# Kernel optimization log

Measured on AMD Instinct MI355X. Metric: run time of the kernel, lower is better.

The kernel has to match this reference:

```python
import jax, jax.numpy as jnp
import numpy as np

B, S, SE, D, H = 4, 1024, 256, 1536, 24
HD = D // H
EPS = 1e-5
STYLE_IDX = np.array([0, 0, 2, 2])  # expand_first: style stats of sample 0 -> {0,1}, sample 2 -> {2,3}


def adain(feat):
    # feat: [B,H,S,hd]; stats over seq dim (-2), unbiased var like torch
    m = feat.mean(axis=-2, keepdims=True)
    s = jnp.sqrt(feat.var(axis=-2, keepdims=True, ddof=1) + EPS)
    sm, ss = m[STYLE_IDX], s[STYLE_IDX]
    styled = (feat - m) / s * ss + sm
    # only batch indices 1 and 3 are restyled
    mask = jnp.array([0.0, 1.0, 0.0, 1.0], dtype=feat.dtype).reshape(B, 1, 1, 1)
    return feat * (1.0 - mask) + styled * mask


def heads(x):
    b, s, _ = x.shape
    return x.reshape(b, s, H, HD).transpose(0, 2, 1, 3)


def setup_inputs() -> dict:
    key = jax.random.key(0)
    ks = jax.random.split(key, 12)
    w = lambda k: jax.random.normal(k, (D, D), dtype=jnp.float32) * 0.02
    z = jnp.zeros((D,), dtype=jnp.float32)
    return {
        'hidden_states': jax.random.normal(ks[0], (B, S, D), dtype=jnp.float32),
        'encoder_hidden_states': jax.random.normal(ks[1], (B, SE, D), dtype=jnp.float32),
        'wq': w(ks[2]), 'bq': z, 'wk': w(ks[3]), 'bk': z, 'wv': w(ks[4]), 'bv': z,
        'awq': w(ks[5]), 'abq': z, 'awk': w(ks[6]), 'abk': z, 'awv': w(ks[7]), 'abv': z,
        'wo': w(ks[8]), 'bo': z, 'wao': w(ks[9]), 'bao': z,
    }


def reference(hidden_states, encoder_hidden_states, wq, bq, wk, bk, wv, bv,
              awq, abq, awk, abk, awv, abv, wo, bo, wao, bao):
    q = heads(hidden_states @ wq + bq)   # [B,H,S,hd]
    k = heads(hidden_states @ wk + bk)
    v = heads(hidden_states @ wv + bv)
    # adain_queries / adain_keys (adain_values=False)
    q = adain(q)
    k = adain(k)
    # share_attention: concat style K/V (scale=1.0 -> plain expand) along seq
    k = jnp.concatenate([k, k[STYLE_IDX]], axis=2)  # [B,H,2S,hd]
    v = jnp.concatenate([v, v[STYLE_IDX]], axis=2)
    # joint (text) streams
    eq = heads(encoder_hidden_states @ awq + abq)
    ek = heads(encoder_hidden_states @ awk + abk)
    ev = heads(encoder_hidden_states @ awv + abv)
    q = jnp.concatenate([q, eq], axis=2)   # [B,H,S+SE,hd]
    k = jnp.concatenate([k, ek], axis=2)   # [B,H,2S+SE,hd]
    v = jnp.concatenate([v, ev], axis=2)
    scale = 1.0 / np.sqrt(HD)
    logits = jnp.einsum('bhqd,bhkd->bhqk', q, k) * scale
    probs = jax.nn.softmax(logits, axis=-1)
    out = jnp.einsum('bhqk,bhkd->bhqd', probs, v)
    out = out.transpose(0, 2, 1, 3).reshape(B, -1, D)
    hid, enc = out[:, :S], out[:, S:]
    hid = hid @ wo + bo            # to_out[0] (to_out[1] is dropout/identity)
    enc = enc @ wao + bao          # to_add_out (context_pre_only=False)
    return hid, enc
```

## Files before the change

kernel.cpp:

```cpp
#include <hip/hip_runtime.h>
#include <hip/hip_bf16.h>


#define NB 4
#define NS 1024
#define NSE 256
#define ND 1536
#define NH 24
#define LK2 1280
#define SMAX 20.0f
#define LOG2E 1.44269504f

typedef short bf16x8 __attribute__((ext_vector_type(8)));
typedef float f32x4 __attribute__((ext_vector_type(4)));

struct WPtrs { const float* w[8]; };
struct B6    { const float* p[6]; };

__device__ __forceinline__ unsigned short f2bf(float x) {
  union { float f; unsigned u; } a; a.f = x;
  unsigned r = a.u + 0x7fffu + ((a.u >> 16) & 1u);
  return (unsigned short)(r >> 16);
}
__device__ __forceinline__ void split2(float x, unsigned short& h, unsigned short& l) {
  union { float f; unsigned u; } a; a.f = x;
  h = (unsigned short)(a.u >> 16);
  union { float f; unsigned u; } b; b.u = a.u & 0xffff0000u;
  union { float f; unsigned u; } c; c.f = x - b.f;
  l = (unsigned short)(c.u >> 16);
}

__device__ __forceinline__ void gload_lds16(const unsigned short* g, unsigned short* l) {
  __builtin_amdgcn_global_load_lds(
      (const __attribute__((address_space(1))) void*)g,
      (__attribute__((address_space(3))) void*)l, 16, 0, 0);
}

__global__ __launch_bounds__(256) void conv_split_all(
    const float* __restrict__ hs, const float* __restrict__ ehs,
    unsigned short* __restrict__ HSh, unsigned short* __restrict__ HSl,
    unsigned short* __restrict__ EHh, unsigned short* __restrict__ EHl)
{
  int i = blockIdx.x * 256 + threadIdx.x;
  const float4* src; ushort4 *dh, *dl; int j;
  if (i < 1572864) { src = (const float4*)hs; j = i; dh = (ushort4*)HSh; dl = (ushort4*)HSl; }
  else { j = i - 1572864; src = (const float4*)ehs; dh = (ushort4*)EHh; dl = (ushort4*)EHl; }
  float4 v = src[j];
  ushort4 h, lo;
  split2(v.x, h.x, lo.x); split2(v.y, h.y, lo.y);
  split2(v.z, h.z, lo.z); split2(v.w, h.w, lo.w);
  dh[j] = h; dl[j] = lo;
}

__global__ __launch_bounds__(256) void conv_wt_all(WPtrs wp,
                                                   unsigned short* __restrict__ Wsp)
{
  __shared__ float tile[32][33];
  const int z = blockIdx.z;
  const float* W = wp.w[z];
  unsigned short* Th = Wsp + (long)(2 * z) * 2359296;
  unsigned short* Tl = Th + 2359296;
  const int k0 = blockIdx.x * 32, n0 = blockIdx.y * 32;
  const int r = threadIdx.x >> 5, c = threadIdx.x & 31;
#pragma unroll
  for (int i = 0; i < 4; ++i)
    tile[r + 8 * i][c] = W[(long)(k0 + r + 8 * i) * ND + n0 + c];
  __syncthreads();
#pragma unroll
  for (int i = 0; i < 4; ++i) {
    float v = tile[c][r + 8 * i];
    long o = (long)(n0 + r + 8 * i) * ND + k0 + c;
    unsigned short h, l;
    split2(v, h, l);
    Th[o] = h; Tl[o] = l;
  }
}

__global__ __launch_bounds__(512, 2) void gemm_qk8(
    const unsigned short* __restrict__ HSh, const unsigned short* __restrict__ EHh,
    const unsigned short* __restrict__ Wsp, B6 biases,
    float* __restrict__ Qb, float* __restrict__ Kb,
    float* __restrict__ EQb, float* __restrict__ EKb)
{
  __shared__ unsigned short sA[2][256 * 32];
  __shared__ unsigned short sBh[2][256 * 32];
  __shared__ unsigned short sBl[2][256 * 32];

  const int lin = blockIdx.x;
  const int idx = (lin & 7) * 30 + (lin >> 3);
  const int z   = idx / 120;
  const int rem = idx % 120;
  const int xn  = rem / 20;
  const int ym  = rem % 20;
  const bool enc = ym >= 16;
  const int m0 = (enc ? (ym - 16) : ym) * 256;
  const int n0 = xn * 256;
  const int widx = z + (enc ? 3 : 0);
  const unsigned short* A  = enc ? EHh : HSh;
  const unsigned short* Bh = Wsp + (long)(2 * widx) * 2359296;
  const unsigned short* Bl = Bh + 2359296;
  float* C = z ? (enc ? EKb : Kb) : (enc ? EQb : Qb);
  const float* bias = biases.p[widx];

  const int t = threadIdx.x, w = t >> 6, l = t & 63;
  const int wm = w >> 2, wn = w & 3;

  const int lrow = l >> 2;
  const int swz  = (l & 3) ^ (lrow & 3);
  const unsigned short* gA0  = A  + (long)(m0 +       w * 16 + lrow) * ND + swz * 8;
  const unsigned short* gA1  = A  + (long)(m0 + 128 + w * 16 + lrow) * ND + swz * 8;
  const unsigned short* gBh0 = Bh + (long)(n0 +       w * 16 + lrow) * ND + swz * 8;
  const unsigned short* gBh1 = Bh + (long)(n0 + 128 + w * 16 + lrow) * ND + swz * 8;
  const unsigned short* gBl0 = Bl + (long)(n0 +       w * 16 + lrow) * ND + swz * 8;
  const unsigned short* gBl1 = Bl + (long)(n0 + 128 + w * 16 + lrow) * ND + swz * 8;

  const int fr = l & 15;
  const int ks = l >> 4;
  const int kx = ((ks ^ (fr & 3)) * 8);

  auto stage = [&](int kt, int bi) {
    const int k0 = kt * 32;
    gload_lds16(gA0  + k0, &sA [bi][(w * 16) * 32]);
    gload_lds16(gA1  + k0, &sA [bi][(128 + w * 16) * 32]);
    gload_lds16(gBh0 + k0, &sBh[bi][(w * 16) * 32]);
    gload_lds16(gBh1 + k0, &sBh[bi][(128 + w * 16) * 32]);
    gload_lds16(gBl0 + k0, &sBl[bi][(w * 16) * 32]);
    gload_lds16(gBl1 + k0, &sBl[bi][(128 + w * 16) * 32]);
  };

  f32x4 acc[8][4] = {};

  stage(0, 0);
  const int NT = ND / 32;
  for (int kt = 0; kt < NT; ++kt) {
    const int cur = kt & 1;
    stage((kt + 1) % NT, cur ^ 1);
    asm volatile("s_waitcnt vmcnt(6)" ::: "memory");
    __builtin_amdgcn_s_barrier();
    __builtin_amdgcn_sched_barrier(0);

    const unsigned short* pA  = &sA[cur][0];
    const unsigned short* pBhc = &sBh[cur][0];
    const unsigned short* pBlc = &sBl[cur][0];

    __builtin_amdgcn_s_setprio(1);
#pragma unroll
    for (int half = 0; half < 2; ++half) {
      bf16x8 fa[4];
#pragma unroll
      for (int a = 0; a < 4; ++a)
        fa[a] = *(const bf16x8*)&pA[(wm * 128 + (half * 4 + a) * 16 + fr) * 32 + kx];
#pragma unroll
      for (int np = 0; np < 2; ++np) {
        bf16x8 fh[2], fl[2];
#pragma unroll
        for (int bq = 0; bq < 2; ++bq) {
          const int col = wn * 64 + (np * 2 + bq) * 16 + fr;
          fh[bq] = *(const bf16x8*)&pBhc[col * 32 + kx];
          fl[bq] = *(const bf16x8*)&pBlc[col * 32 + kx];
        }
#pragma unroll
        for (int a = 0; a < 4; ++a)
#pragma unroll
          for (int bq = 0; bq < 2; ++bq) {
            acc[half * 4 + a][np * 2 + bq] = __builtin_amdgcn_mfma_f32_16x16x32_bf16(
                fa[a], fh[bq], acc[half * 4 + a][np * 2 + bq], 0, 0, 0);
            acc[half * 4 + a][np * 2 + bq] = __builtin_amdgcn_mfma_f32_16x16x32_bf16(
                fa[a], fl[bq], acc[half * 4 + a][np * 2 + bq], 0, 0, 0);
          }
      }
    }
    __builtin_amdgcn_s_setprio(0);

    asm volatile("s_waitcnt lgkmcnt(0)" ::: "memory");
    __builtin_amdgcn_sched_barrier(0);
    __builtin_amdgcn_s_barrier();
  }

  const int col0 = n0 + wn * 64 + fr;
  const int row0 = m0 + wm * 128 + ks * 4;
#pragma unroll
  for (int ni = 0; ni < 4; ++ni) {
    float bv = bias[col0 + ni * 16];
#pragma unroll
    for (int mi = 0; mi < 8; ++mi)
#pragma unroll
      for (int r = 0; r < 4; ++r)
        C[(long)(row0 + mi * 16 + r) * ND + col0 + ni * 16] = acc[mi][ni][r] + bv;
  }
}

__device__ __forceinline__ void gemm_mfma_body(
    const unsigned short* __restrict__ Ah, const unsigned short* __restrict__ Al,
    const unsigned short* __restrict__ Bh, const unsigned short* __restrict__ Bl,
    const float* __restrict__ bias, float* __restrict__ C, int m0, int n0,
    bool third)
{
  __shared__ unsigned short sAh[128 * 32], sAl[128 * 32];
  __shared__ unsigned short sBh[128 * 32], sBl[128 * 32];

  const int t = threadIdx.x;
  const int w = t >> 6, l = t & 63;

  const int lr = l >> 2;
  const int lc = (l & 3) * 8;

  const unsigned short* pAh = Ah + (long)(m0 + 32 * w + lr) * ND + lc;
  const unsigned short* pAl = Al + (long)(m0 + 32 * w + lr) * ND + lc;
  const unsigned short* pBh = Bh + (long)(n0 + 32 * w + lr) * ND + lc;
  const unsigned short* pBl = Bl + (long)(n0 + 32 * w + lr) * ND + lc;

  unsigned short* qAh0 = &sAh[(32 * w) * 32];
  unsigned short* qAh1 = &sAh[(32 * w + 16) * 32];
  unsigned short* qAl0 = &sAl[(32 * w) * 32];
  unsigned short* qAl1 = &sAl[(32 * w + 16) * 32];
  unsigned short* qBh0 = &sBh[(32 * w) * 32];
  unsigned short* qBh1 = &sBh[(32 * w + 16) * 32];
  unsigned short* qBl0 = &sBl[(32 * w) * 32];
  unsigned short* qBl1 = &sBl[(32 * w + 16) * 32];

  const int rowA = (w >> 1) * 64 + (l & 15);
  const int rowB = (w & 1) * 64 + (l & 15);
  const int ko = (l >> 4) * 8;

  f32x4 acc[4][4] = {};

  for (int k0 = 0; k0 < ND; k0 += 32) {
    gload_lds16(pAh, qAh0);
    gload_lds16(pAh + 16 * ND, qAh1);
    if (third) {
      gload_lds16(pAl, qAl0);
      gload_lds16(pAl + 16 * ND, qAl1);
    }
    gload_lds16(pBh, qBh0);
    gload_lds16(pBh + 16 * ND, qBh1);
    gload_lds16(pBl, qBl0);
    gload_lds16(pBl + 16 * ND, qBl1);
    pAh += 32; pAl += 32; pBh += 32; pBl += 32;
    __syncthreads();

    bf16x8 fah[4], fal[4], fbh[4], fbl[4];
#pragma unroll
    for (int mt = 0; mt < 4; ++mt)
      fah[mt] = *(const bf16x8*)&sAh[(rowA + mt * 16) * 32 + ko];
    if (third) {
#pragma unroll
      for (int mt = 0; mt < 4; ++mt)
        fal[mt] = *(const bf16x8*)&sAl[(rowA + mt * 16) * 32 + ko];
    }
#pragma unroll
    for (int nt = 0; nt < 4; ++nt) {
      fbh[nt] = *(const bf16x8*)&sBh[(rowB + nt * 16) * 32 + ko];
      fbl[nt] = *(const bf16x8*)&sBl[(rowB + nt * 16) * 32 + ko];
    }
#pragma unroll
    for (int mt = 0; mt < 4; ++mt)
#pragma unroll
      for (int nt = 0; nt < 4; ++nt) {
        acc[mt][nt] = __builtin_amdgcn_mfma_f32_16x16x32_bf16(fah[mt], fbh[nt], acc[mt][nt], 0, 0, 0);
        acc[mt][nt] = __builtin_amdgcn_mfma_f32_16x16x32_bf16(fah[mt], fbl[nt], acc[mt][nt], 0, 0, 0);
      }
    if (third) {
#pragma unroll
      for (int mt = 0; mt < 4; ++mt)
#pragma unroll
        for (int nt = 0; nt < 4; ++nt)
          acc[mt][nt] = __builtin_amdgcn_mfma_f32_16x16x32_bf16(fal[mt], fbh[nt], acc[mt][nt], 0, 0, 0);
    }
    __syncthreads();
  }

  const int col0 = n0 + (w & 1) * 64 + (l & 15);
  const int row0 = m0 + (w >> 1) * 64 + (l >> 4) * 4;
#pragma unroll
  for (int nt = 0; nt < 4; ++nt) {
    float bv = bias[col0 + nt * 16];
#pragma unroll
    for (int mt = 0; mt < 4; ++mt)
#pragma unroll
      for (int r = 0; r < 4; ++r)
        C[(long)(row0 + mt * 16 + r) * ND + col0 + nt * 16] = acc[mt][nt][r] + bv;
  }
}

__global__ __launch_bounds__(256) void gemm_v_all(
    const unsigned short* __restrict__ HSh, const unsigned short* __restrict__ HSl,
    const unsigned short* __restrict__ EHh, const unsigned short* __restrict__ EHl,
    const unsigned short* __restrict__ Wsp, B6 biases,
    float* __restrict__ Vb, float* __restrict__ EVb)
{
  const int y = blockIdx.y;
  const unsigned short *Ah, *Al;
  float* C;
  int m0, widx;
  if (y < 32) { Ah = HSh; Al = HSl; m0 = y * 128; widx = 2; C = Vb; }
  else        { Ah = EHh; Al = EHl; m0 = (y - 32) * 128; widx = 5; C = EVb; }
  const unsigned short* Bh = Wsp + (long)(2 * widx) * 2359296;
  const unsigned short* Bl = Bh + 2359296;
  gemm_mfma_body(Ah, Al, Bh, Bl, biases.p[widx], C, m0, blockIdx.x * 128, true);
}

__global__ __launch_bounds__(256) void gemm_out_all(
    const unsigned short* __restrict__ AOh,
    const unsigned short* __restrict__ Wsp,
    const float* __restrict__ bo, const float* __restrict__ bao,
    float* __restrict__ out)
{
  const int z = blockIdx.z, y = blockIdx.y;
  const unsigned short *Ah, *Bh, *Bl;
  const float* bias;
  float* C;
  int m0;
  if (y < 8) {
    Ah = AOh + (long)z * 1966080;
    m0 = y * 128;
    Bh = Wsp + (long)12 * 2359296; Bl = Bh + 2359296;
    bias = bo; C = out + (long)z * 1572864;
  } else {
    Ah = AOh + 1572864 + (long)z * 1966080;
    m0 = (y - 8) * 128;
    Bh = Wsp + (long)14 * 2359296; Bl = Bh + 2359296;
    bias = bao; C = out + 6291456 + (long)z * 393216;
  }
  gemm_mfma_body(Ah, Ah, Bh, Bl, bias, C, m0, blockIdx.x * 128, false);
}

__global__ __launch_bounds__(256) void adain_stats2(
    const float* __restrict__ Qb, const float* __restrict__ Kb,
    float* __restrict__ stm, float* __restrict__ sts,
    float* __restrict__ stm2, float* __restrict__ sts2)
{
  const float* X = blockIdx.z ? Kb : Qb;
  float* meanb = blockIdx.z ? stm2 : stm;
  float* sigb  = blockIdx.z ? sts2 : sts;
  const int b  = blockIdx.x;
  const int t  = threadIdx.x;
  const int dl = t & 63;
  const int sg = t >> 6;
  const int d  = blockIdx.y * 64 + dl;
  const float* xp = X + (long)b * NS * ND + d;
  float sum = 0.f, sq = 0.f;
  for (int s = sg; s < NS; s += 4) {
    float v = xp[(long)s * ND];
    sum += v; sq += v * v;
  }
  __shared__ float ss[4][64], s2[4][64];
  ss[sg][dl] = sum; s2[sg][dl] = sq;
  __syncthreads();
  if (t < 64) {
    float tot = ss[0][t] + ss[1][t] + ss[2][t] + ss[3][t];
    float tq  = s2[0][t] + s2[1][t] + s2[2][t] + s2[3][t];
    float mean = tot * (1.f / 1024.f);
    float var  = (tq - tot * mean) * (1.f / 1023.f);
    meanb[b * ND + blockIdx.y * 64 + t] = mean;
    sigb [b * ND + blockIdx.y * 64 + t] = sqrtf(var + 1e-5f);
  }
}

__global__ __launch_bounds__(256) void conv_KV(
    const float* __restrict__ Kf, const float* __restrict__ EKf,
    const float* __restrict__ Vf, const float* __restrict__ EVf,
    const float* __restrict__ stm2, const float* __restrict__ sts2,
    unsigned short* __restrict__ Kh, unsigned short* __restrict__ Kl,
    unsigned short* __restrict__ VT)
{
  __shared__ float tile[64][65];
  const int bh = blockIdx.y, b = bh / NH, h = bh - b * NH;
  if (blockIdx.x < 20) {
    const int key = blockIdx.x * 64 + (threadIdx.x >> 2);
    const int dc = (threadIdx.x & 3) * 16;
    const bool kad = ((b & 1) != 0) && (key < NS);
    const int srcb = b & 2;
    const float* src = (key < NS)
        ? Kf  + ((long)b * NS + key) * ND + h * 64 + dc
        : EKf + ((long)b * NSE + key - NS) * ND + h * 64 + dc;
    unsigned short* dh = Kh + ((long)bh * LK2 + key) * 64 + dc;
    unsigned short* dl = Kl + ((long)bh * LK2 + key) * 64 + dc;
    const long sb = (long)b * ND + h * 64 + dc;
    const long ss = (long)srcb * ND + h * 64 + dc;
#pragma unroll
    for (int i = 0; i < 4; ++i) {
      float4 v = *(const float4*)(src + 4 * i);
      if (kad) {
        float4 mb = *(const float4*)(stm2 + sb + 4 * i);
        float4 gb = *(const float4*)(sts2 + sb + 4 * i);
        float4 ms = *(const float4*)(stm2 + ss + 4 * i);
        float4 gs = *(const float4*)(sts2 + ss + 4 * i);
        v.x = (v.x - mb.x) * (gs.x / gb.x) + ms.x;
        v.y = (v.y - mb.y) * (gs.y / gb.y) + ms.y;
        v.z = (v.z - mb.z) * (gs.z / gb.z) + ms.z;
        v.w = (v.w - mb.w) * (gs.w / gb.w) + ms.w;
      }
      ushort4 hi, lo;
      split2(v.x, hi.x, lo.x); split2(v.y, hi.y, lo.y);
      split2(v.z, hi.z, lo.z); split2(v.w, hi.w, lo.w);
      *(ushort4*)(dh + 4 * i) = hi;
      *(ushort4*)(dl + 4 * i) = lo;
    }
  } else {
    const int k0 = (blockIdx.x - 20) * 64;
    {
      const int kl_ = threadIdx.x >> 2, dc = (threadIdx.x & 3) * 16;
      const int key = k0 + kl_;
      const float* src = (key < NS)
          ? Vf  + ((long)b * NS + key) * ND + h * 64 + dc
          : EVf + ((long)b * NSE + key - NS) * ND + h * 64 + dc;
#pragma unroll
      for (int i = 0; i < 4; ++i) {
        float4 v = *(const float4*)(src + 4 * i);
        tile[kl_][dc + 4 * i + 0] = v.x; tile[kl_][dc + 4 * i + 1] = v.y;
        tile[kl_][dc + 4 * i + 2] = v.z; tile[kl_][dc + 4 * i + 3] = v.w;
      }
    }
    __syncthreads();
    const int d = threadIdx.x >> 2, kc = (threadIdx.x & 3) * 16;
    unsigned short* dst = VT + ((long)bh * 64 + d) * LK2 + k0 + kc;
#pragma unroll
    for (int i = 0; i < 4; ++i) {
      ushort4 o4;
      o4.x = f2bf(tile[kc + 4 * i + 0][d]);
      o4.y = f2bf(tile[kc + 4 * i + 1][d]);
      o4.z = f2bf(tile[kc + 4 * i + 2][d]);
      o4.w = f2bf(tile[kc + 4 * i + 3][d]);
      *(ushort4*)(dst + 4 * i) = o4;
    }
  }
}

__global__ __launch_bounds__(256, 4) void attn_mfma(
    const float* __restrict__ Q, const float* __restrict__ EQ,
    const unsigned short* __restrict__ Khg, const unsigned short* __restrict__ Klg,
    const unsigned short* __restrict__ VTg,
    const float* __restrict__ stm, const float* __restrict__ sts,
    unsigned short* __restrict__ AOh)
{
  __shared__ unsigned short sKh[2][32 * 64], sKl[2][32 * 64], sVT[2][64 * 32];
  __shared__ unsigned short sPh[64 * 40], sPl[64 * 40];

  const int t = threadIdx.x, w = t >> 6, l = t & 63;
  const int x = blockIdx.x & 7;
  const int u = blockIdx.x >> 3;
  const int i6 = 6 * x + u / 20;
  const int q0 = (u % 20) * 64;
  const int m = l & 15, g = l >> 4;

  const int srow = l >> 3, sp = l & 7;
  const int offK = (8 * w + srow) * 64 + ((sp - srow) & 7) * 8;
  const int dv = l >> 2, cv = l & 3;
  const int vrow = 16 * w + dv;
  const int vcol = ((cv - ((dv + (dv >> 2)) & 3)) & 3) * 8;
  const int rfm = (m + (m >> 2)) & 3;

  const int p0 = (g + m) & 7;
  const int p1 = (4 + g + m) & 7;

  union FU { bf16x8 v; unsigned short u[8]; };

  for (int seg = 0; seg < 2; ++seg) {
    const int bh = seg ? (i6 < 24 ? i6 + 24 : i6 + 48)
                       : (i6 < 24 ? i6      : i6 + 24);
    const int b = bh / NH, h = bh - b * NH;
    const int bhs = (b & 2) * NH + h;
    const bool beven = (seg == 0);
    const int nIter = beven ? 40 : 72;

    FU qh[2], ql[2];
    {
      const bool qad = !beven && (q0 < NS);
      const int srcb = b & 2;
      const float* qrow = (q0 < NS)
          ? (Q  + ((long)b * NS + q0 + 16 * w + m) * ND + h * 64)
          : (EQ + ((long)b * NSE + (q0 - NS) + 16 * w + m) * ND + h * 64);
#pragma unroll
      for (int ks = 0; ks < 2; ++ks) {
        const int d0 = h * 64 + ks * 32 + g * 8;
        const float* p = qrow + ks * 32 + g * 8;
        float4 v0 = *(const float4*)p, v1 = *(const float4*)(p + 4);
        float vv[8] = {v0.x, v0.y, v0.z, v0.w, v1.x, v1.y, v1.z, v1.w};
        if (qad) {
          float4 mb0 = *(const float4*)(stm + (long)b * ND + d0);
          float4 mb1 = *(const float4*)(stm + (long)b * ND + d0 + 4);
          float4 gb0 = *(const float4*)(sts + (long)b * ND + d0);
          float4 gb1 = *(const float4*)(sts + (long)b * ND + d0 + 4);
          float4 ms0 = *(const float4*)(stm + (long)srcb * ND + d0);
          float4 ms1 = *(const float4*)(stm + (long)srcb * ND + d0 + 4);
          float4 gs0 = *(const float4*)(sts + (long)srcb * ND + d0);
          float4 gs1 = *(const float4*)(sts + (long)srcb * ND + d0 + 4);
          float mb[8] = {mb0.x, mb0.y, mb0.z, mb0.w, mb1.x, mb1.y, mb1.z, mb1.w};
          float gb[8] = {gb0.x, gb0.y, gb0.z, gb0.w, gb1.x, gb1.y, gb1.z, gb1.w};
          float ms[8] = {ms0.x, ms0.y, ms0.z, ms0.w, ms1.x, ms1.y, ms1.z, ms1.w};
          float gs[8] = {gs0.x, gs0.y, gs0.z, gs0.w, gs1.x, gs1.y, gs1.z, gs1.w};
#pragma unroll
          for (int j2 = 0; j2 < 8; ++j2)
            vv[j2] = (vv[j2] - mb[j2]) * (gs[j2] / gb[j2]) + ms[j2];
        }
#pragma unroll
        for (int j2 = 0; j2 < 8; ++j2)
          split2(vv[j2] * (0.125f * LOG2E), qh[ks].u[j2], ql[ks].u[j2]);
      }
    }

    const long ownK = (long)bh * LK2 * 64, styK = (long)bhs * LK2 * 64;
    const long ownV = (long)bh * 64 * LK2, styV = (long)bhs * 64 * LK2;

    auto stage = [&](int kt, int bi) {
      int zone, jz;
      if (beven) { zone = (kt < 32) ? 0 : 2; jz = (kt < 32) ? kt : kt - 32; }
      else {
        zone = (kt < 32) ? 0 : ((kt < 64) ? 1 : 2);
        jz = (kt < 32) ? kt : ((kt < 64) ? kt - 32 : kt - 64);
      }
      const long keyBase = ((zone == 2) ? 1024 : 0) + (long)jz * 32;
      const unsigned short* kb = Khg + ((zone == 1) ? styK : ownK) + keyBase * 64;
      const unsigned short* lb = Klg + ((zone == 1) ? styK : ownK) + keyBase * 64;
      const unsigned short* vb = VTg + ((zone == 1) ? styV : ownV) + keyBase;
      gload_lds16(kb + offK, &sKh[bi][(8 * w) * 64]);
      gload_lds16(lb + offK, &sKl[bi][(8 * w) * 64]);
      gload_lds16(vb + (long)vrow * LK2 + vcol, &sVT[bi][(16 * w) * 32]);
    };

    f32x4 oacc[4] = {};
    float l_part[4] = {0.f, 0.f, 0.f, 0.f};

    stage(0, 0);

    for (int kt = 0; kt < nIter; ++kt) {
      const int cur = kt & 1;
      __syncthreads();
      if (kt + 1 < nIter) stage(kt + 1, cur ^ 1);

      const float ebias = (beven && kt < 32) ? (1.0f - SMAX * LOG2E)
                                             : (-SMAX * LOG2E);

      f32x4 sacc[2] = {};
      __builtin_amdgcn_s_setprio(1);
#pragma unroll
      for (int ks = 0; ks < 2; ++ks) {
        const int pp = ks ? p1 : p0;
#pragma unroll
        for (int nt = 0; nt < 2; ++nt) {
          const int ak = (nt * 16 + m) * 64 + pp * 8;
          bf16x8 fkh = *(const bf16x8*)&sKh[cur][ak];
          bf16x8 fkl = *(const bf16x8*)&sKl[cur][ak];
          sacc[nt] = __builtin_amdgcn_mfma_f32_16x16x32_bf16(qh[ks].v, fkh, sacc[nt], 0, 0, 0);
          sacc[nt] = __builtin_amdgcn_mfma_f32_16x16x32_bf16(qh[ks].v, fkl, sacc[nt], 0, 0, 0);
          sacc[nt] = __builtin_amdgcn_mfma_f32_16x16x32_bf16(ql[ks].v, fkh, sacc[nt], 0, 0, 0);
        }
      }
      __builtin_amdgcn_s_setprio(0);

#pragma unroll
      for (int nt = 0; nt < 2; ++nt)
#pragma unroll
        for (int r = 0; r < 4; ++r)
          sacc[nt][r] = __builtin_amdgcn_exp2f(sacc[nt][r] + ebias);
#pragma unroll
      for (int r = 0; r < 4; ++r)
        l_part[r] += sacc[0][r] + sacc[1][r];
#pragma unroll
      for (int nt = 0; nt < 2; ++nt)
#pragma unroll
        for (int r = 0; r < 4; ++r) {
          unsigned short ph, pl;
          split2(sacc[nt][r], ph, pl);
          const int ad = (16 * w + 4 * g + r) * 40 + nt * 16 + m;
          sPh[ad] = ph; sPl[ad] = pl;
        }

      __builtin_amdgcn_s_setprio(1);
      {
        const int ap = (16 * w + m) * 40 + g * 8;
        bf16x8 fph = *(const bf16x8*)&sPh[ap];
        bf16x8 fpl = *(const bf16x8*)&sPl[ap];
#pragma unroll
        for (int nt2 = 0; nt2 < 4; ++nt2) {
          const int av = (nt2 * 16 + m) * 32 + ((g + rfm) & 3) * 8;
          bf16x8 fv = *(const bf16x8*)&sVT[cur][av];
          oacc[nt2] = __builtin_amdgcn_mfma_f32_16x16x32_bf16(fph, fv, oacc[nt2], 0, 0, 0);
          oacc[nt2] = __builtin_amdgcn_mfma_f32_16x16x32_bf16(fpl, fv, oacc[nt2], 0, 0, 0);
        }
      }
      __builtin_amdgcn_s_setprio(0);
    }

#pragma unroll
    for (int r = 0; r < 4; ++r) {
#pragma unroll
      for (int off = 1; off < 16; off <<= 1)
        l_part[r] += __shfl_xor(l_part[r], off, 16);
    }
#pragma unroll
    for (int r = 0; r < 4; ++r) {
      float inv = 1.f / l_part[r];
      const long row = (long)b * 1280 + q0 + 16 * w + 4 * g + r;
      const long base = row * ND + h * 64;
#pragma unroll
      for (int nt2 = 0; nt2 < 4; ++nt2)
        AOh[base + nt2 * 16 + m] = f2bf(oacc[nt2][r] * inv);
    }
  }
}

extern "C" void kernel_launch(void* const* d_in, const int* in_sizes, int n_in,
                              void* d_out, int out_size, void* d_ws, size_t ws_size,
                              hipStream_t stream) {
  const float* hs  = (const float*)d_in[0];
  const float* ehs = (const float*)d_in[1];
  WPtrs wp;
  wp.w[0] = (const float*)d_in[2];  wp.w[1] = (const float*)d_in[4];
  wp.w[2] = (const float*)d_in[6];  wp.w[3] = (const float*)d_in[8];
  wp.w[4] = (const float*)d_in[10]; wp.w[5] = (const float*)d_in[12];
  wp.w[6] = (const float*)d_in[14]; wp.w[7] = (const float*)d_in[16];
  B6 biases;
  biases.p[0] = (const float*)d_in[3];
  biases.p[1] = (const float*)d_in[5];
  biases.p[2] = (const float*)d_in[7];
  biases.p[3] = (const float*)d_in[9];
  biases.p[4] = (const float*)d_in[11];
  biases.p[5] = (const float*)d_in[13];
  const float* bo  = (const float*)d_in[15];
  const float* bao = (const float*)d_in[17];
  float* out = (float*)d_out;

  float* Qb  = (float*)d_ws;
  float* Kb  = Qb  + 6291456;
  float* Vb  = Kb  + 6291456;
  float* EQb = Vb  + 6291456;
  float* EKb = EQb + 1572864;
  float* EVb = EKb + 1572864;
  float* stm  = EVb + 1572864;
  float* sts  = stm + 6144;
  float* stm2 = sts + 6144;
  float* sts2 = stm2 + 6144;
  unsigned short* U0  = (unsigned short*)(sts2 + 6144);
  unsigned short* HSh = U0;
  unsigned short* HSl = U0 + 6291456;
  unsigned short* EHh = U0 + 12582912;
  unsigned short* EHl = U0 + 14155776;
  unsigned short* AOh = U0;
  unsigned short* Wsp = U0 + 15728640;
  unsigned short* Khg = Wsp;
  unsigned short* Klg = Wsp + 7864320;
  unsigned short* VTg = Wsp + 15728640;

  dim3 blk(256);

  conv_split_all<<<7680, blk, 0, stream>>>(hs, ehs, HSh, HSl, EHh, EHl);
  conv_wt_all<<<dim3(48, 48, 8), blk, 0, stream>>>(wp, Wsp);

  gemm_qk8<<<240, 512, 0, stream>>>(HSh, EHh, Wsp, biases, Qb, Kb, EQb, EKb);
  gemm_v_all<<<dim3(12, 40), blk, 0, stream>>>(HSh, HSl, EHh, EHl, Wsp, biases,
                                               Vb, EVb);

  adain_stats2<<<dim3(4, 24, 2), blk, 0, stream>>>(Qb, Kb, stm, sts, stm2, sts2);

  conv_KV<<<dim3(40, 96), blk, 0, stream>>>(Kb, EKb, Vb, EVb, stm2, sts2,
                                            Khg, Klg, VTg);

  attn_mfma<<<dim3(960), blk, 0, stream>>>(Qb, EQb, Khg, Klg, VTg,
                                           stm, sts, AOh);

  gemm_out_all<<<dim3(12, 10, 4), blk, 0, stream>>>(AOh, Wsp, bo, bao, out);
}
```

Baseline: 702.4 us.

## Triple-buffer QK projection GEMM with interleaved prefetch and swizzle P tile

The fp32-split QK projection GEMM moves from double to triple buffering in LDS. Its K-step is split into four MFMA phases, with the A, Bh and Bl global-to-LDS loads for tile kt+2 spread between them. This aims to hide global load latency and overlap LDS fragment reads with MFMA work, at the cost of more barriers per iteration and 50% more shared memory, which may cut occupancy. Separately, the attention kernel's probability tile in LDS gets an XOR swizzle on its 8-element blocks, aiming to reduce bank conflicts on the scatter writes and vector reads.

```diff
diff --git a/kernel.cpp b/kernel.cpp
--- a/kernel.cpp
+++ b/kernel.cpp
@@ -10,6 +10,7 @@
 #define LK2 1280
 #define SMAX 20.0f
 #define LOG2E 1.44269504f
+#define SPW 40
 
 typedef short bf16x8 __attribute__((ext_vector_type(8)));
 typedef float f32x4 __attribute__((ext_vector_type(4)));
@@ -82,9 +83,9 @@
     float* __restrict__ Qb, float* __restrict__ Kb,
     float* __restrict__ EQb, float* __restrict__ EKb)
 {
-  __shared__ unsigned short sA[2][256 * 32];
-  __shared__ unsigned short sBh[2][256 * 32];
-  __shared__ unsigned short sBl[2][256 * 32];
+  __shared__ unsigned short sA[3][256 * 32];
+  __shared__ unsigned short sBh[3][256 * 32];
+  __shared__ unsigned short sBl[3][256 * 32];
 
   const int lin = blockIdx.x;
   const int idx = (lin & 7) * 30 + (lin >> 3);
@@ -118,7 +119,7 @@
   const int ks = l >> 4;
   const int kx = ((ks ^ (fr & 3)) * 8);
 
-  auto stage = [&](int kt, int bi) {
+  auto stage6 = [&](int kt, int bi) {
     const int k0 = kt * 32;
     gload_lds16(gA0  + k0, &sA [bi][(w * 16) * 32]);
     gload_lds16(gA1  + k0, &sA [bi][(128 + w * 16) * 32]);
@@ -130,50 +131,106 @@
 
   f32x4 acc[8][4] = {};
 
-  stage(0, 0);
+  stage6(0, 0);
+  stage6(1, 1);
+  asm volatile("s_waitcnt vmcnt(6)" ::: "memory");
+  __builtin_amdgcn_s_barrier();
+
   const int NT = ND / 32;
   for (int kt = 0; kt < NT; ++kt) {
-    const int cur = kt & 1;
-    stage((kt + 1) % NT, cur ^ 1);
-    asm volatile("s_waitcnt vmcnt(6)" ::: "memory");
-    __builtin_amdgcn_s_barrier();
-    __builtin_amdgcn_sched_barrier(0);
-
-    const unsigned short* pA  = &sA[cur][0];
+    const int cur = kt % 3;
+    const unsigned short* pA   = &sA [cur][0];
     const unsigned short* pBhc = &sBh[cur][0];
     const unsigned short* pBlc = &sBl[cur][0];
-
+    const bool pf = (kt + 2 < NT);
+    const int nb = (kt + 2) % 3;
+    const int nk0 = (kt + 2) * 32;
+
+    bf16x8 fa[4], fh0[2], fl0[2], fh1[2], fl1[2];
+
+#pragma unroll
+    for (int a = 0; a < 4; ++a)
+      fa[a] = *(const bf16x8*)&pA[(wm * 128 + a * 16 + fr) * 32 + kx];
+#pragma unroll
+    for (int bq = 0; bq < 2; ++bq) {
+      const int col = wn * 64 + bq * 16 + fr;
+      fh0[bq] = *(const bf16x8*)&pBhc[col * 32 + kx];
+      fl0[bq] = *(const bf16x8*)&pBlc[col * 32 + kx];
+    }
+    if (pf) {
+      gload_lds16(gA0 + nk0, &sA[nb][(w * 16) * 32]);
+      gload_lds16(gA1 + nk0, &sA[nb][(128 + w * 16) * 32]);
+    }
+    __builtin_amdgcn_s_barrier();
+    asm volatile("s_waitcnt lgkmcnt(0)");
+    __builtin_amdgcn_sched_barrier(0);
     __builtin_amdgcn_s_setprio(1);
 #pragma unroll
-    for (int half = 0; half < 2; ++half) {
-      bf16x8 fa[4];
-#pragma unroll
-      for (int a = 0; a < 4; ++a)
-        fa[a] = *(const bf16x8*)&pA[(wm * 128 + (half * 4 + a) * 16 + fr) * 32 + kx];
-#pragma unroll
-      for (int np = 0; np < 2; ++np) {
-        bf16x8 fh[2], fl[2];
-#pragma unroll
-        for (int bq = 0; bq < 2; ++bq) {
-          const int col = wn * 64 + (np * 2 + bq) * 16 + fr;
-          fh[bq] = *(const bf16x8*)&pBhc[col * 32 + kx];
-          fl[bq] = *(const bf16x8*)&pBlc[col * 32 + kx];
-        }
-#pragma unroll
-        for (int a = 0; a < 4; ++a)
-#pragma unroll
-          for (int bq = 0; bq < 2; ++bq) {
-            acc[half * 4 + a][np * 2 + bq] = __builtin_amdgcn_mfma_f32_16x16x32_bf16(
-                fa[a], fh[bq], acc[half * 4 + a][np * 2 + bq], 0, 0, 0);
-            acc[half * 4 + a][np * 2 + bq] = __builtin_amdgcn_mfma_f32_16x16x32_bf16(
-                fa[a], fl[bq], acc[half * 4 + a][np * 2 + bq], 0, 0, 0);
-          }
-      }
-    }
+    for (int a = 0; a < 4; ++a)
+#pragma unroll
+      for (int bq = 0; bq < 2; ++bq) {
+        acc[a][bq] = __builtin_amdgcn_mfma_f32_16x16x32_bf16(fa[a], fh0[bq], acc[a][bq], 0, 0, 0);
+        acc[a][bq] = __builtin_amdgcn_mfma_f32_16x16x32_bf16(fa[a], fl0[bq], acc[a][bq], 0, 0, 0);
+      }
     __builtin_amdgcn_s_setprio(0);
-
-    asm volatile("s_waitcnt lgkmcnt(0)" ::: "memory");
+    __builtin_amdgcn_s_barrier();
+
+#pragma unroll
+    for (int bq = 0; bq < 2; ++bq) {
+      const int col = wn * 64 + (2 + bq) * 16 + fr;
+      fh1[bq] = *(const bf16x8*)&pBhc[col * 32 + kx];
+      fl1[bq] = *(const bf16x8*)&pBlc[col * 32 + kx];
+    }
+    if (pf) {
+      gload_lds16(gBh0 + nk0, &sBh[nb][(w * 16) * 32]);
+      gload_lds16(gBh1 + nk0, &sBh[nb][(128 + w * 16) * 32]);
+    }
+    __builtin_amdgcn_s_barrier();
+    asm volatile("s_waitcnt lgkmcnt(0)");
     __builtin_amdgcn_sched_barrier(0);
+    __builtin_amdgcn_s_setprio(1);
+#pragma unroll
+    for (int a = 0; a < 4; ++a)
+#pragma unroll
+      for (int bq = 0; bq < 2; ++bq) {
+        acc[a][2 + bq] = __builtin_amdgcn_mfma_f32_16x16x32_bf16(fa[a], fh1[bq], acc[a][2 + bq], 0, 0, 0);
+        acc[a][2 + bq] = __builtin_amdgcn_mfma_f32_16x16x32_bf16(fa[a], fl1[bq], acc[a][2 + bq], 0, 0, 0);
+      }
+    __builtin_amdgcn_s_setprio(0);
+    __builtin_amdgcn_s_barrier();
+
+#pragma unroll
+    for (int a = 0; a < 4; ++a)
+      fa[a] = *(const bf16x8*)&pA[(wm * 128 + (4 + a) * 16 + fr) * 32 + kx];
+    if (pf) {
+      gload_lds16(gBl0 + nk0, &sBl[nb][(w * 16) * 32]);
+      gload_lds16(gBl1 + nk0, &sBl[nb][(128 + w * 16) * 32]);
+    }
+    __builtin_amdgcn_s_barrier();
+    asm volatile("s_waitcnt lgkmcnt(0)");
+    __builtin_amdgcn_sched_barrier(0);
+    __builtin_amdgcn_s_setprio(1);
+#pragma unroll
+    for (int a = 0; a < 4; ++a)
+#pragma unroll
+      for (int bq = 0; bq < 2; ++bq) {
+        acc[4 + a][bq] = __builtin_amdgcn_mfma_f32_16x16x32_bf16(fa[a], fh0[bq], acc[4 + a][bq], 0, 0, 0);
+        acc[4 + a][bq] = __builtin_amdgcn_mfma_f32_16x16x32_bf16(fa[a], fl0[bq], acc[4 + a][bq], 0, 0, 0);
+      }
+    __builtin_amdgcn_s_setprio(0);
+    __builtin_amdgcn_s_barrier();
+
+    __builtin_amdgcn_s_setprio(1);
+#pragma unroll
+    for (int a = 0; a < 4; ++a)
+#pragma unroll
+      for (int bq = 0; bq < 2; ++bq) {
+        acc[4 + a][2 + bq] = __builtin_amdgcn_mfma_f32_16x16x32_bf16(fa[a], fh1[bq], acc[4 + a][2 + bq], 0, 0, 0);
+        acc[4 + a][2 + bq] = __builtin_amdgcn_mfma_f32_16x16x32_bf16(fa[a], fl1[bq], acc[4 + a][2 + bq], 0, 0, 0);
+      }
+    __builtin_amdgcn_s_setprio(0);
+    if (pf) asm volatile("s_waitcnt vmcnt(6)" ::: "memory");
+    else    asm volatile("s_waitcnt vmcnt(0)" ::: "memory");
     __builtin_amdgcn_s_barrier();
   }
 
@@ -435,7 +492,7 @@
     unsigned short* __restrict__ AOh)
 {
   __shared__ unsigned short sKh[2][32 * 64], sKl[2][32 * 64], sVT[2][64 * 32];
-  __shared__ unsigned short sPh[64 * 40], sPl[64 * 40];
+  __shared__ unsigned short sPh[64 * SPW], sPl[64 * SPW];
 
   const int t = threadIdx.x, w = t >> 6, l = t & 63;
   const int x = blockIdx.x & 7;
@@ -563,13 +620,16 @@
         for (int r = 0; r < 4; ++r) {
           unsigned short ph, pl;
           split2(sacc[nt][r], ph, pl);
-          const int ad = (16 * w + 4 * g + r) * 40 + nt * 16 + m;
+          const int row = 16 * w + 4 * g + r;
+          const int blk = nt * 2 + (m >> 3);
+          const int ad = row * SPW + ((blk ^ g) << 3) + (m & 7);
           sPh[ad] = ph; sPl[ad] = pl;
         }
 
       __builtin_amdgcn_s_setprio(1);
       {
-        const int ap = (16 * w + m) * 40 + g * 8;
+        const int prow = 16 * w + m;
+        const int ap = prow * SPW + ((g ^ ((m >> 2) & 3)) << 3);
         bf16x8 fph = *(const bf16x8*)&sPh[ap];
         bf16x8 fpl = *(const bf16x8*)&sPl[ap];
 #pragma unroll
```

Result: no change. 689.8 us (-1.8%).
